# Optimization experiments

Measured on AMD Instinct MI355X. Metric: run time of the kernel, lower is better.

The kernel has to match this reference:

```python
import jax, jax.numpy as jnp
import numpy as np

BATCH_SIZE = 2048
INPUT_AXIS = 3
A = BATCH_SIZE * INPUT_AXIS          # 6144
C = BATCH_SIZE * INPUT_AXIS          # 6144 (A == B == C)
D = BATCH_SIZE * (INPUT_AXIS - 1)    # 4096


def _linear_init(key, fan_out, fan_in):
    kw, kb = jax.random.split(key)
    bound = 1.0 / np.sqrt(fan_in)
    W = jax.random.uniform(kw, (fan_out, fan_in), jnp.float32, -bound, bound)
    b = jax.random.uniform(kb, (fan_out,), jnp.float32, -bound, bound)
    return W, b


def setup_inputs() -> dict:
    key = jax.random.key(0)
    ks = jax.random.split(key, 8)
    x = jax.random.normal(ks[0], (A,), jnp.float32)
    dims = [(C, A), (C, C), (C, C), (C, C), (C, C), (C, C), (D, C)]
    inp = {"x": x}
    for i, (fo, fi) in enumerate(dims):
        W, b = _linear_init(ks[i + 1], fo, fi)
        inp[f"W{i+1}"] = W
        inp[f"b{i+1}"] = b
    return inp


def _pairwise_flat(data, offset):
    # cord[n] = offset + data[n]; dist[n,m] = ||cord[n]-cord[m]||_2, flattened row-major.
    cord = offset + data                        # [B, d]
    diff = cord[:, None, :] - cord[None, :, :]  # [B, B, d]
    d2 = jnp.sum(diff * diff, axis=-1)          # [B, B]
    # safe sqrt: zero distance (diagonal) -> 0 with zero gradient
    safe = jnp.where(d2 > 0, d2, 1.0)
    dist = jnp.where(d2 > 0, jnp.sqrt(safe), 0.0)
    return dist.reshape(-1)                     # [B*B]


def reference(x, W1, b1, W2, b2, W3, b3, W4, b4, W5, b5, W6, b6, W7, b7):
    h = x
    for W, b in ((W1, b1), (W2, b2), (W3, b3), (W4, b4), (W5, b5), (W6, b6)):
        h = jax.nn.relu(h @ W.T + b)
    z = h @ W7.T + b7
    y = z * jax.nn.sigmoid(z)  # Swish

    in_data = x.reshape(BATCH_SIZE, INPUT_AXIS)
    lat_repr = y.reshape(BATCH_SIZE, INPUT_AXIS - 1)
    in_min = jnp.min(in_data)
    lat_min = jnp.min(lat_repr)

    in_diff_sum = _pairwise_flat(in_data, in_min)
    lat_diff_sum = _pairwise_flat(lat_repr, lat_min)
    return (in_diff_sum, lat_diff_sum, lat_repr)
```

## Files before the change

### kernel.cpp

```cpp
#include <hip/hip_runtime.h>
#include <math.h>


#define K_DIM 6144
#define NV    (K_DIM / 4)
#define WITER (NV / 64)

template<bool RELU>
__global__ __launch_bounds__(256) void gemv_k6144(
    const float* __restrict__ W, const float* __restrict__ b,
    const float* __restrict__ x, float* __restrict__ out, int nRows)
{
    __shared__ float4 xs[NV];

    const float4* __restrict__ xg = (const float4*)x;
#pragma unroll
    for (int i = 0; i < NV / 256; ++i)
        xs[i * 256 + threadIdx.x] = xg[i * 256 + threadIdx.x];
    __syncthreads();

    const int gwave = (blockIdx.x * 256 + threadIdx.x) >> 6;
    const int lane  = threadIdx.x & 63;
    if (gwave >= nRows) return;

    const float4* __restrict__ Wr = (const float4*)(W + (size_t)gwave * K_DIM);

    float4 w[WITER];
#pragma unroll
    for (int i = 0; i < WITER; ++i)
        w[i] = Wr[i * 64 + lane];

    float a0 = 0.f, a1 = 0.f, a2 = 0.f, a3 = 0.f;
#pragma unroll
    for (int i = 0; i < WITER; ++i) {
        float4 v = xs[i * 64 + lane];
        a0 = fmaf(w[i].x, v.x, a0);
        a1 = fmaf(w[i].y, v.y, a1);
        a2 = fmaf(w[i].z, v.z, a2);
        a3 = fmaf(w[i].w, v.w, a3);
    }
    float acc = (a0 + a1) + (a2 + a3);

#pragma unroll
    for (int off = 32; off > 0; off >>= 1)
        acc += __shfl_down(acc, off, 64);

    if (lane == 0) {
        float z = acc + b[gwave];
        float r;
        if (RELU) {
            r = fmaxf(z, 0.f);
        } else {
            r = z / (1.f + expf(-z));
        }
        out[gwave] = r;
    }
}

__global__ __launch_bounds__(256) void pdist3_kernel(
    const float* __restrict__ x, float* __restrict__ out)
{
    const int idx = blockIdx.x * 256 + threadIdx.x;
    const int n = idx >> 11;
    const int m = idx & 2047;
    float a0 = x[3 * n + 0], a1 = x[3 * n + 1], a2 = x[3 * n + 2];
    float c0 = x[3 * m + 0], c1 = x[3 * m + 1], c2 = x[3 * m + 2];
    float d0 = a0 - c0, d1 = a1 - c1, d2 = a2 - c2;
    float s = d0 * d0 + d1 * d1 + d2 * d2;
    out[idx] = (s > 0.f) ? sqrtf(s) : 0.f;
}

__global__ __launch_bounds__(256) void pdist2_kernel(
    const float* __restrict__ y, float* __restrict__ out)
{
    const int idx = blockIdx.x * 256 + threadIdx.x;
    const int n = idx >> 11;
    const int m = idx & 2047;
    float a0 = y[2 * n + 0], a1 = y[2 * n + 1];
    float c0 = y[2 * m + 0], c1 = y[2 * m + 1];
    float d0 = a0 - c0, d1 = a1 - c1;
    float s = d0 * d0 + d1 * d1;
    out[idx] = (s > 0.f) ? sqrtf(s) : 0.f;
}

extern "C" void kernel_launch(void* const* d_in, const int* in_sizes, int n_in,
                              void* d_out, int out_size, void* d_ws, size_t ws_size,
                              hipStream_t stream)
{
    const float* x  = (const float*)d_in[0];
    const float* W1 = (const float*)d_in[1];   const float* b1 = (const float*)d_in[2];
    const float* W2 = (const float*)d_in[3];   const float* b2 = (const float*)d_in[4];
    const float* W3 = (const float*)d_in[5];   const float* b3 = (const float*)d_in[6];
    const float* W4 = (const float*)d_in[7];   const float* b4 = (const float*)d_in[8];
    const float* W5 = (const float*)d_in[9];   const float* b5 = (const float*)d_in[10];
    const float* W6 = (const float*)d_in[11];  const float* b6 = (const float*)d_in[12];
    const float* W7 = (const float*)d_in[13];  const float* b7 = (const float*)d_in[14];

    float* out      = (float*)d_out;
    float* in_dist  = out;
    float* lat_dist = out + 2048 * 2048;
    float* y        = out + 2 * 2048 * 2048;

    float* hA = (float*)d_ws;
    float* hB = hA + K_DIM;

    const int BS = 256;
    const int g6144 = 6144 / 4;
    const int g4096 = 4096 / 4;
    const int gPD   = (2048 * 2048) / BS;

    pdist3_kernel<<<gPD, BS, 0, stream>>>(x, in_dist);

    gemv_k6144<true ><<<g6144, BS, 0, stream>>>(W1, b1, x,  hA, 6144);
    gemv_k6144<true ><<<g6144, BS, 0, stream>>>(W2, b2, hA, hB, 6144);
    gemv_k6144<true ><<<g6144, BS, 0, stream>>>(W3, b3, hB, hA, 6144);
    gemv_k6144<true ><<<g6144, BS, 0, stream>>>(W4, b4, hA, hB, 6144);
    gemv_k6144<true ><<<g6144, BS, 0, stream>>>(W5, b5, hB, hA, 6144);
    gemv_k6144<true ><<<g6144, BS, 0, stream>>>(W6, b6, hA, hB, 6144);
    gemv_k6144<false><<<g4096, BS, 0, stream>>>(W7, b7, hB, y,  4096);

    pdist2_kernel<<<gPD, BS, 0, stream>>>(y, lat_dist);
}
```

Before: 796.7 us.

## Fuse seven GEMV layers into one persistent kernel with grid barriers

Replaces the seven separate GEMV launches with a single persistent kernel of 512 blocks that loops over layers. Waves grid-stride over output rows, and an atomic counter barrier per layer synchronises all blocks before the next layer reads the activations. This removes six kernel launches and their inter-kernel gaps. In exchange it adds spin-wait barriers and needs all 512 blocks to be co-resident, otherwise it deadlocks. Each wave now handles several rows, which may lower memory-level parallelism on the weight stream.

```diff
diff --git a/kernel.cpp b/kernel.cpp
--- a/kernel.cpp
+++ b/kernel.cpp
@@ -2,58 +2,88 @@
 #include <math.h>
 
 
-#define K_DIM 6144
-#define NV    (K_DIM / 4)
-#define WITER (NV / 64)
+#define K_DIM   6144
+#define NV      (K_DIM / 4)
+#define WITER   24
+#define NBLOCKS 512
+#define NWAVES  (NBLOCKS * 4)
 
-template<bool RELU>
-__global__ __launch_bounds__(256) void gemv_k6144(
-    const float* __restrict__ W, const float* __restrict__ b,
-    const float* __restrict__ x, float* __restrict__ out, int nRows)
+struct Params {
+    const float* W[7];
+    const float* b[7];
+    const float* x;
+    float*       act0;
+    float*       act1;
+    float*       y;
+    unsigned int* bar;
+};
+
+__global__ __launch_bounds__(256, 2) void mlp_fused(Params p)
 {
     __shared__ float4 xs[NV];
 
-    const float4* __restrict__ xg = (const float4*)x;
+    const int wid  = threadIdx.x >> 6;
+    const int lane = threadIdx.x & 63;
+    const int gw   = blockIdx.x * 4 + wid;
+
+    const float* in = p.x;
+
+    for (int L = 0; L < 7; ++L) {
+        const float4* __restrict__ ing = (const float4*)in;
+        for (int i = threadIdx.x; i < NV; i += 256)
+            xs[i] = ing[i];
+        __syncthreads();
+
+        const int nRows = (L == 6) ? 4096 : 6144;
+        float* outp = (L == 6) ? p.y : ((L & 1) ? p.act1 : p.act0);
+        const float* __restrict__ bias = p.b[L];
+
+        for (int r = gw; r < nRows; r += NWAVES) {
+            const float4* __restrict__ Wr =
+                (const float4*)(p.W[L] + (size_t)r * K_DIM);
+
+            float4 w[WITER];
 #pragma unroll
-    for (int i = 0; i < NV / 256; ++i)
-        xs[i * 256 + threadIdx.x] = xg[i * 256 + threadIdx.x];
-    __syncthreads();
+            for (int i = 0; i < WITER; ++i)
+                w[i] = Wr[i * 64 + lane];
 
-    const int gwave = (blockIdx.x * 256 + threadIdx.x) >> 6;
-    const int lane  = threadIdx.x & 63;
-    if (gwave >= nRows) return;
+            float a0 = 0.f, a1 = 0.f, a2 = 0.f, a3 = 0.f;
+#pragma unroll
+            for (int i = 0; i < WITER; ++i) {
+                float4 v = xs[i * 64 + lane];
+                a0 = fmaf(w[i].x, v.x, a0);
+                a1 = fmaf(w[i].y, v.y, a1);
+                a2 = fmaf(w[i].z, v.z, a2);
+                a3 = fmaf(w[i].w, v.w, a3);
+            }
+            float acc = (a0 + a1) + (a2 + a3);
+#pragma unroll
+            for (int off = 32; off > 0; off >>= 1)
+                acc += __shfl_down(acc, off, 64);
 
-    const float4* __restrict__ Wr = (const float4*)(W + (size_t)gwave * K_DIM);
+            if (lane == 0) {
+                float z = acc + bias[r];
+                outp[r] = (L < 6) ? fmaxf(z, 0.f)
+                                  : z / (1.f + expf(-z));
+            }
+        }
 
-    float4 w[WITER];
-#pragma unroll
-    for (int i = 0; i < WITER; ++i)
-        w[i] = Wr[i * 64 + lane];
-
-    float a0 = 0.f, a1 = 0.f, a2 = 0.f, a3 = 0.f;
-#pragma unroll
-    for (int i = 0; i < WITER; ++i) {
-        float4 v = xs[i * 64 + lane];
-        a0 = fmaf(w[i].x, v.x, a0);
-        a1 = fmaf(w[i].y, v.y, a1);
-        a2 = fmaf(w[i].z, v.z, a2);
-        a3 = fmaf(w[i].w, v.w, a3);
-    }
-    float acc = (a0 + a1) + (a2 + a3);
-
-#pragma unroll
-    for (int off = 32; off > 0; off >>= 1)
-        acc += __shfl_down(acc, off, 64);
-
-    if (lane == 0) {
-        float z = acc + b[gwave];
-        float r;
-        if (RELU) {
-            r = fmaxf(z, 0.f);
-        } else {
-            r = z / (1.f + expf(-z));
+        if (L < 6) {
+            __syncthreads();
+            __threadfence();
+            __syncthreads();
+            if (threadIdx.x == 0) {
+                __hip_atomic_fetch_add(&p.bar[L], 1u,
+                                       __ATOMIC_RELEASE, __HIP_MEMORY_SCOPE_AGENT);
+                while (__hip_atomic_load(&p.bar[L],
+                                         __ATOMIC_ACQUIRE, __HIP_MEMORY_SCOPE_AGENT)
+                       < (unsigned)NBLOCKS)
+                    __builtin_amdgcn_s_sleep(2);
+            }
+            __syncthreads();
+            __threadfence();
+            in = (L & 1) ? p.act1 : p.act0;
         }
-        out[gwave] = r;
     }
 }
 
@@ -87,37 +117,34 @@
                               void* d_out, int out_size, void* d_ws, size_t ws_size,
                               hipStream_t stream)
 {
-    const float* x  = (const float*)d_in[0];
-    const float* W1 = (const float*)d_in[1];   const float* b1 = (const float*)d_in[2];
-    const float* W2 = (const float*)d_in[3];   const float* b2 = (const float*)d_in[4];
-    const float* W3 = (const float*)d_in[5];   const float* b3 = (const float*)d_in[6];
-    const float* W4 = (const float*)d_in[7];   const float* b4 = (const float*)d_in[8];
-    const float* W5 = (const float*)d_in[9];   const float* b5 = (const float*)d_in[10];
-    const float* W6 = (const float*)d_in[11];  const float* b6 = (const float*)d_in[12];
-    const float* W7 = (const float*)d_in[13];  const float* b7 = (const float*)d_in[14];
+    const float* x = (const float*)d_in[0];
+
+    Params p;
+    for (int i = 0; i < 7; ++i) {
+        p.W[i] = (const float*)d_in[1 + 2 * i];
+        p.b[i] = (const float*)d_in[2 + 2 * i];
+    }
+    p.x = x;
 
     float* out      = (float*)d_out;
     float* in_dist  = out;
     float* lat_dist = out + 2048 * 2048;
     float* y        = out + 2 * 2048 * 2048;
 
-    float* hA = (float*)d_ws;
-    float* hB = hA + K_DIM;
+    float* ws = (float*)d_ws;
+    p.act0 = ws;
+    p.act1 = ws + K_DIM;
+    p.y    = y;
+    p.bar  = (unsigned int*)(ws + 2 * K_DIM);
 
-    const int BS = 256;
-    const int g6144 = 6144 / 4;
-    const int g4096 = 4096 / 4;
-    const int gPD   = (2048 * 2048) / BS;
+    hipMemsetAsync(p.bar, 0, 8 * sizeof(unsigned int), stream);
+
+    const int BS  = 256;
+    const int gPD = (2048 * 2048) / BS;
 
     pdist3_kernel<<<gPD, BS, 0, stream>>>(x, in_dist);
 
-    gemv_k6144<true ><<<g6144, BS, 0, stream>>>(W1, b1, x,  hA, 6144);
-    gemv_k6144<true ><<<g6144, BS, 0, stream>>>(W2, b2, hA, hB, 6144);
-    gemv_k6144<true ><<<g6144, BS, 0, stream>>>(W3, b3, hB, hA, 6144);
-    gemv_k6144<true ><<<g6144, BS, 0, stream>>>(W4, b4, hA, hB, 6144);
-    gemv_k6144<true ><<<g6144, BS, 0, stream>>>(W5, b5, hB, hA, 6144);
-    gemv_k6144<true ><<<g6144, BS, 0, stream>>>(W6, b6, hA, hB, 6144);
-    gemv_k6144<false><<<g4096, BS, 0, stream>>>(W7, b7, hB, y,  4096);
+    mlp_fused<<<NBLOCKS, BS, 0, stream>>>(p);
 
     pdist2_kernel<<<gPD, BS, 0, stream>>>(y, lat_dist);
 }
```

After: 1.525 ms. 1.91x slower.
